# Kernel optimization log

Hardware: AMD Instinct MI355X
Metric: run time of the kernel (lower is better)

Reference implementation:

```python
import jax, jax.numpy as jnp
import numpy as np

TAU = 0.05
SIGMA = 0.05
THETA = 1.0
MAX_ITER = 30
B, N, M1, M2 = 8192, 256, 128, 64


def setup_inputs() -> dict:
    key = jax.random.key(0)
    k = jax.random.split(key, 5)
    x0 = jax.random.normal(k[0], (B, N), dtype=jnp.float32)
    y1_0 = jnp.zeros((B, M1), dtype=jnp.float32)
    y2_0 = jnp.zeros((B, M2), dtype=jnp.float32)
    z = jax.random.normal(k[1], (B, M1 + M2), dtype=jnp.float32)
    c = jax.random.normal(k[2], (N,), dtype=jnp.float32)
    # scale constraint matrices so tau*sigma*||A||^2 < 1 (PDHG stability)
    A1 = jax.random.normal(k[3], (M1, N), dtype=jnp.float32) * 0.1
    A2 = jax.random.normal(k[4], (M2, N), dtype=jnp.float32) * 0.1
    return {"x0": x0, "y1_0": y1_0, "y2_0": y2_0, "z": z, "c": c, "A1": A1, "A2": A2}


def reference(x0, y1_0, y2_0, z, c, A1, A2):
    # affine constraint maps: ineq_map(x, z) = x @ A1^T - z1 ; eq_map(x, z) = x @ A2^T - z2
    # adjoints: A1^T y1 = y1 @ A1 ; A2^T y2 = y2 @ A2
    # prox: projection onto nonnegative orthant
    z1, z2 = z[:, :M1], z[:, M1:]

    def step(carry, _):
        x, x_bar, y1, y2 = carry
        y1 = jnp.maximum(y1 + SIGMA * (x_bar @ A1.T - z1), 0.0)   # dual ineq ascent + clamp
        y2 = y2 + SIGMA * (x_bar @ A2.T - z2)                     # dual eq ascent
        grad = c + y1 @ A1 + y2 @ A2                              # [B, N] via broadcast of c
        x_next = jnp.maximum(x - TAU * grad, 0.0)                 # prox (nonneg projection)
        x_bar = x_next + THETA * (x_next - x)                     # extrapolation
        return (x_next, x_bar, y1, y2), None

    (x, _, y1, y2), _ = jax.lax.scan(step, (x0, x0, y1_0, y2_0), None, length=MAX_ITER)
    return (x, y1, y2)
```

## Files before the change

### kernel.cpp

```cpp
#include <hip/hip_runtime.h>

typedef __attribute__((ext_vector_type(8))) __bf16 bf16x8;
typedef __attribute__((ext_vector_type(4))) float f32x4;

constexpr int Bn = 8192, Nn = 256, M1n = 128, M2n = 64, Mn = 192, ITERS = 30;
constexpr float TAUc = 0.05f, SIGc = 0.05f;

__device__ __forceinline__ ushort f2bf(float f) {
  unsigned u = __builtin_bit_cast(unsigned, f);
  u = (u + 0x7FFFu + ((u >> 16) & 1u)) >> 16;
  return (ushort)u;
}

__global__ void prep_kernel(const float* __restrict__ A1, const float* __restrict__ A2,
                            ushort* __restrict__ Arm, ushort* __restrict__ AT) {
  int i = blockIdx.x * 256 + threadIdx.x;
  if (i >= Mn * Nn) return;
  int m = i / Nn, n = i % Nn;
  float v = (m < M1n) ? A1[m * Nn + n] : A2[(m - M1n) * Nn + n];
  ushort b = f2bf(v);
  Arm[m * Nn + n] = b;
  AT[n * Mn + m] = b;
}

__global__ __launch_bounds__(512, 2) void pdhg_kernel(
    const float* __restrict__ x0, const float* __restrict__ y10,
    const float* __restrict__ y20, const float* __restrict__ z,
    const float* __restrict__ c, const ushort* __restrict__ Arm,
    const ushort* __restrict__ AT, float* __restrict__ out) {
  __shared__ __align__(16) ushort xb_lds[16][264];
  __shared__ __align__(16) ushort y_lds[16][200];

  const int lane = threadIdx.x & 63;
  const int w = threadIdx.x >> 6;
  const int fr = lane & 15;
  const int kg = lane >> 4;
  const int row0 = blockIdx.x * 16;

  const int nt0 = 2 * w;
  const int mt0 = w;
  const bool two_m = (w < 4);
  const int mt1 = two_m ? (8 + w) : w;
  const int m0 = mt0 * 16 + fr;
  const int m1 = mt1 * 16 + fr;

  float x[2][4], cv[2];
  float y0s[4], z0s[4], y1s[4], z1s[4];

#pragma unroll
  for (int t = 0; t < 2; ++t) {
    int n = (nt0 + t) * 16 + fr;
    cv[t] = c[n];
#pragma unroll
    for (int g = 0; g < 4; ++g) {
      float v = x0[(row0 + kg * 4 + g) * Nn + n];
      x[t][g] = v;
      xb_lds[kg * 4 + g][n] = f2bf(v);
    }
  }
#pragma unroll
  for (int g = 0; g < 4; ++g) {
    int r = row0 + kg * 4 + g;
    z0s[g] = z[r * Mn + m0];
    y0s[g] = y10[r * M1n + m0];
    z1s[g] = z[r * Mn + m1];
    y1s[g] = two_m ? y20[r * M2n + (m1 - M1n)] : 0.f;
  }

  bf16x8 armF0[8], armF1[8], atF[2][6];
#pragma unroll
  for (int kf = 0; kf < 8; ++kf) {
    armF0[kf] = *reinterpret_cast<const bf16x8*>(&Arm[m0 * Nn + kf * 32 + kg * 8]);
    armF1[kf] = *reinterpret_cast<const bf16x8*>(&Arm[m1 * Nn + kf * 32 + kg * 8]);
  }
#pragma unroll
  for (int t = 0; t < 2; ++t)
#pragma unroll
    for (int kf = 0; kf < 6; ++kf)
      atF[t][kf] = *reinterpret_cast<const bf16x8*>(&AT[((nt0 + t) * 16 + fr) * Mn + kf * 32 + kg * 8]);

  __syncthreads();

  for (int it = 0; it < ITERS; ++it) {
    bf16x8 fx[8];
#pragma unroll
    for (int kf = 0; kf < 8; ++kf)
      fx[kf] = *reinterpret_cast<const bf16x8*>(&xb_lds[fr][kf * 32 + kg * 8]);

    f32x4 a0 = {0.f, 0.f, 0.f, 0.f}, a1 = {0.f, 0.f, 0.f, 0.f};
    if (two_m) {
#pragma unroll
      for (int kf = 0; kf < 8; ++kf) {
        a0 = __builtin_amdgcn_mfma_f32_16x16x32_bf16(fx[kf], armF0[kf], a0, 0, 0, 0);
        a1 = __builtin_amdgcn_mfma_f32_16x16x32_bf16(fx[kf], armF1[kf], a1, 0, 0, 0);
      }
    } else {
#pragma unroll
      for (int kf = 0; kf < 8; ++kf)
        a0 = __builtin_amdgcn_mfma_f32_16x16x32_bf16(fx[kf], armF0[kf], a0, 0, 0, 0);
    }

#pragma unroll
    for (int g = 0; g < 4; ++g) {
      float s = fmaxf(y0s[g] + SIGc * (a0[g] - z0s[g]), 0.f);
      y0s[g] = s;
      y_lds[kg * 4 + g][m0] = f2bf(s);
    }
    if (two_m) {
#pragma unroll
      for (int g = 0; g < 4; ++g) {
        float s = y1s[g] + SIGc * (a1[g] - z1s[g]);
        y1s[g] = s;
        y_lds[kg * 4 + g][m1] = f2bf(s);
      }
    }
    __syncthreads();

    bf16x8 fy[6];
#pragma unroll
    for (int kf = 0; kf < 6; ++kf)
      fy[kf] = *reinterpret_cast<const bf16x8*>(&y_lds[fr][kf * 32 + kg * 8]);

    f32x4 b0 = {0.f, 0.f, 0.f, 0.f}, b1 = {0.f, 0.f, 0.f, 0.f};
#pragma unroll
    for (int kf = 0; kf < 6; ++kf) {
      b0 = __builtin_amdgcn_mfma_f32_16x16x32_bf16(fy[kf], atF[0][kf], b0, 0, 0, 0);
      b1 = __builtin_amdgcn_mfma_f32_16x16x32_bf16(fy[kf], atF[1][kf], b1, 0, 0, 0);
    }

    const bool notlast = (it != ITERS - 1);
#pragma unroll
    for (int t = 0; t < 2; ++t) {
      int n = (nt0 + t) * 16 + fr;
      f32x4 bb = t ? b1 : b0;
#pragma unroll
      for (int g = 0; g < 4; ++g) {
        float grad = cv[t] + bb[g];
        float xn = fmaxf(x[t][g] - TAUc * grad, 0.f);
        float xb = 2.f * xn - x[t][g];
        x[t][g] = xn;
        if (notlast) xb_lds[kg * 4 + g][n] = f2bf(xb);
      }
    }
    __syncthreads();
  }

  float* ox = out;
  float* oy1 = out + Bn * Nn;
  float* oy2 = oy1 + Bn * M1n;
#pragma unroll
  for (int t = 0; t < 2; ++t) {
    int n = (nt0 + t) * 16 + fr;
#pragma unroll
    for (int g = 0; g < 4; ++g)
      ox[(row0 + kg * 4 + g) * Nn + n] = x[t][g];
  }
#pragma unroll
  for (int g = 0; g < 4; ++g) {
    int r = row0 + kg * 4 + g;
    oy1[r * M1n + m0] = y0s[g];
  }
  if (two_m) {
#pragma unroll
    for (int g = 0; g < 4; ++g) {
      int r = row0 + kg * 4 + g;
      oy2[r * M2n + (m1 - M1n)] = y1s[g];
    }
  }
}

extern "C" void kernel_launch(void* const* d_in, const int* in_sizes, int n_in,
                              void* d_out, int out_size, void* d_ws, size_t ws_size,
                              hipStream_t stream) {
  const float* x0  = (const float*)d_in[0];
  const float* y10 = (const float*)d_in[1];
  const float* y20 = (const float*)d_in[2];
  const float* z   = (const float*)d_in[3];
  const float* c   = (const float*)d_in[4];
  const float* A1  = (const float*)d_in[5];
  const float* A2  = (const float*)d_in[6];

  ushort* Arm = (ushort*)d_ws;
  ushort* AT  = Arm + Mn * Nn;

  prep_kernel<<<(Mn * Nn + 255) / 256, 256, 0, stream>>>(A1, A2, Arm, AT);
  pdhg_kernel<<<Bn / 16, 512, 0, stream>>>(x0, y10, y20, z, c, Arm, AT, (float*)d_out);
}
```

Baseline: 79.95 us.

## Use 4 waves per block with balanced MFMA tiles and packed bf16 conversion

```diff
diff --git a/kernel.cpp b/kernel.cpp
--- a/kernel.cpp
+++ b/kernel.cpp
@@ -12,6 +12,12 @@
   return (ushort)u;
 }
 
+__device__ __forceinline__ unsigned cvtpk(float lo, float hi) {
+  unsigned r;
+  asm("v_cvt_pk_bf16_f32 %0, %1, %2" : "=v"(r) : "v"(lo), "v"(hi));
+  return r;
+}
+
 __global__ void prep_kernel(const float* __restrict__ A1, const float* __restrict__ A2,
                             ushort* __restrict__ Arm, ushort* __restrict__ AT) {
   int i = blockIdx.x * 256 + threadIdx.x;
@@ -23,13 +29,14 @@
   AT[n * Mn + m] = b;
 }
 
-__global__ __launch_bounds__(512, 2) void pdhg_kernel(
+__global__ __launch_bounds__(256, 2) void pdhg_kernel(
     const float* __restrict__ x0, const float* __restrict__ y10,
     const float* __restrict__ y20, const float* __restrict__ z,
     const float* __restrict__ c, const ushort* __restrict__ Arm,
     const ushort* __restrict__ AT, float* __restrict__ out) {
   __shared__ __align__(16) ushort xb_lds[16][264];
   __shared__ __align__(16) ushort y_lds[16][200];
+  __shared__ __align__(16) float z_lds[16][200];
 
   const int lane = threadIdx.x & 63;
   const int w = threadIdx.x >> 6;
@@ -37,19 +44,16 @@
   const int kg = lane >> 4;
   const int row0 = blockIdx.x * 16;
 
-  const int nt0 = 2 * w;
-  const int mt0 = w;
-  const bool two_m = (w < 4);
-  const int mt1 = two_m ? (8 + w) : w;
-  const int m0 = mt0 * 16 + fr;
-  const int m1 = mt1 * 16 + fr;
+  for (int idx = threadIdx.x; idx < 16 * Mn; idx += 256) {
+    int r = idx / Mn, m = idx - r * Mn;
+    z_lds[r][m] = SIGc * z[(row0 + r) * Mn + m];
+  }
 
-  float x[2][4], cv[2];
-  float y0s[4], z0s[4], y1s[4], z1s[4];
+  float x[4][4], cv[4], ys[3][4];
 
 #pragma unroll
-  for (int t = 0; t < 2; ++t) {
-    int n = (nt0 + t) * 16 + fr;
+  for (int t = 0; t < 4; ++t) {
+    int n = (4 * w + t) * 16 + fr;
     cv[t] = c[n];
 #pragma unroll
     for (int g = 0; g < 4; ++g) {
@@ -59,112 +63,117 @@
     }
   }
 #pragma unroll
-  for (int g = 0; g < 4; ++g) {
-    int r = row0 + kg * 4 + g;
-    z0s[g] = z[r * Mn + m0];
-    y0s[g] = y10[r * M1n + m0];
-    z1s[g] = z[r * Mn + m1];
-    y1s[g] = two_m ? y20[r * M2n + (m1 - M1n)] : 0.f;
+  for (int i = 0; i < 3; ++i) {
+    int mt = 3 * w + i;
+    int m = mt * 16 + fr;
+#pragma unroll
+    for (int g = 0; g < 4; ++g) {
+      int r = row0 + kg * 4 + g;
+      ys[i][g] = (m < M1n) ? y10[r * M1n + m] : y20[r * M2n + (m - M1n)];
+    }
   }
 
-  bf16x8 armF0[8], armF1[8], atF[2][6];
+  bf16x8 armF[3][8], atF[4][6];
 #pragma unroll
-  for (int kf = 0; kf < 8; ++kf) {
-    armF0[kf] = *reinterpret_cast<const bf16x8*>(&Arm[m0 * Nn + kf * 32 + kg * 8]);
-    armF1[kf] = *reinterpret_cast<const bf16x8*>(&Arm[m1 * Nn + kf * 32 + kg * 8]);
+  for (int i = 0; i < 3; ++i) {
+    int m = (3 * w + i) * 16 + fr;
+#pragma unroll
+    for (int kf = 0; kf < 8; ++kf)
+      armF[i][kf] = *reinterpret_cast<const bf16x8*>(&Arm[m * Nn + kf * 32 + kg * 8]);
   }
 #pragma unroll
-  for (int t = 0; t < 2; ++t)
+  for (int t = 0; t < 4; ++t) {
+    int n = (4 * w + t) * 16 + fr;
 #pragma unroll
     for (int kf = 0; kf < 6; ++kf)
-      atF[t][kf] = *reinterpret_cast<const bf16x8*>(&AT[((nt0 + t) * 16 + fr) * Mn + kf * 32 + kg * 8]);
+      atF[t][kf] = *reinterpret_cast<const bf16x8*>(&AT[n * Mn + kf * 32 + kg * 8]);
+  }
 
   __syncthreads();
 
   for (int it = 0; it < ITERS; ++it) {
-    bf16x8 fx[8];
+    f32x4 a0 = {0.f, 0.f, 0.f, 0.f}, a1 = a0, a2 = a0;
 #pragma unroll
-    for (int kf = 0; kf < 8; ++kf)
-      fx[kf] = *reinterpret_cast<const bf16x8*>(&xb_lds[fr][kf * 32 + kg * 8]);
-
-    f32x4 a0 = {0.f, 0.f, 0.f, 0.f}, a1 = {0.f, 0.f, 0.f, 0.f};
-    if (two_m) {
-#pragma unroll
-      for (int kf = 0; kf < 8; ++kf) {
-        a0 = __builtin_amdgcn_mfma_f32_16x16x32_bf16(fx[kf], armF0[kf], a0, 0, 0, 0);
-        a1 = __builtin_amdgcn_mfma_f32_16x16x32_bf16(fx[kf], armF1[kf], a1, 0, 0, 0);
-      }
-    } else {
-#pragma unroll
-      for (int kf = 0; kf < 8; ++kf)
-        a0 = __builtin_amdgcn_mfma_f32_16x16x32_bf16(fx[kf], armF0[kf], a0, 0, 0, 0);
+    for (int kf = 0; kf < 8; ++kf) {
+      bf16x8 fx = *reinterpret_cast<const bf16x8*>(&xb_lds[fr][kf * 32 + kg * 8]);
+      a0 = __builtin_amdgcn_mfma_f32_16x16x32_bf16(fx, armF[0][kf], a0, 0, 0, 0);
+      a1 = __builtin_amdgcn_mfma_f32_16x16x32_bf16(fx, armF[1][kf], a1, 0, 0, 0);
+      a2 = __builtin_amdgcn_mfma_f32_16x16x32_bf16(fx, armF[2][kf], a2, 0, 0, 0);
     }
 
 #pragma unroll
-    for (int g = 0; g < 4; ++g) {
-      float s = fmaxf(y0s[g] + SIGc * (a0[g] - z0s[g]), 0.f);
-      y0s[g] = s;
-      y_lds[kg * 4 + g][m0] = f2bf(s);
-    }
-    if (two_m) {
+    for (int i = 0; i < 3; ++i) {
+      int mt = 3 * w + i;
+      int m = mt * 16 + fr;
+      const f32x4 ai = (i == 0) ? a0 : (i == 1) ? a1 : a2;
 #pragma unroll
       for (int g = 0; g < 4; ++g) {
-        float s = y1s[g] + SIGc * (a1[g] - z1s[g]);
-        y1s[g] = s;
-        y_lds[kg * 4 + g][m1] = f2bf(s);
+        float s = __builtin_fmaf(SIGc, ai[g], ys[i][g]) - z_lds[kg * 4 + g][m];
+        if (mt < 8) s = fmaxf(s, 0.f);
+        ys[i][g] = s;
       }
+      unsigned p01 = cvtpk(ys[i][0], ys[i][1]);
+      unsigned p23 = cvtpk(ys[i][2], ys[i][3]);
+      y_lds[kg * 4 + 0][m] = (ushort)p01;
+      y_lds[kg * 4 + 1][m] = (ushort)(p01 >> 16);
+      y_lds[kg * 4 + 2][m] = (ushort)p23;
+      y_lds[kg * 4 + 3][m] = (ushort)(p23 >> 16);
     }
     __syncthreads();
 
-    bf16x8 fy[6];
-#pragma unroll
-    for (int kf = 0; kf < 6; ++kf)
-      fy[kf] = *reinterpret_cast<const bf16x8*>(&y_lds[fr][kf * 32 + kg * 8]);
-
-    f32x4 b0 = {0.f, 0.f, 0.f, 0.f}, b1 = {0.f, 0.f, 0.f, 0.f};
+    f32x4 b0 = {0.f, 0.f, 0.f, 0.f}, b1 = b0, b2 = b0, b3 = b0;
 #pragma unroll
     for (int kf = 0; kf < 6; ++kf) {
-      b0 = __builtin_amdgcn_mfma_f32_16x16x32_bf16(fy[kf], atF[0][kf], b0, 0, 0, 0);
-      b1 = __builtin_amdgcn_mfma_f32_16x16x32_bf16(fy[kf], atF[1][kf], b1, 0, 0, 0);
+      bf16x8 fy = *reinterpret_cast<const bf16x8*>(&y_lds[fr][kf * 32 + kg * 8]);
+      b0 = __builtin_amdgcn_mfma_f32_16x16x32_bf16(fy, atF[0][kf], b0, 0, 0, 0);
+      b1 = __builtin_amdgcn_mfma_f32_16x16x32_bf16(fy, atF[1][kf], b1, 0, 0, 0);
+      b2 = __builtin_amdgcn_mfma_f32_16x16x32_bf16(fy, atF[2][kf], b2, 0, 0, 0);
+      b3 = __builtin_amdgcn_mfma_f32_16x16x32_bf16(fy, atF[3][kf], b3, 0, 0, 0);
     }
 
     const bool notlast = (it != ITERS - 1);
 #pragma unroll
-    for (int t = 0; t < 2; ++t) {
-      int n = (nt0 + t) * 16 + fr;
-      f32x4 bb = t ? b1 : b0;
+    for (int t = 0; t < 4; ++t) {
+      int n = (4 * w + t) * 16 + fr;
+      const f32x4 bt = (t == 0) ? b0 : (t == 1) ? b1 : (t == 2) ? b2 : b3;
+      float xb[4];
 #pragma unroll
       for (int g = 0; g < 4; ++g) {
-        float grad = cv[t] + bb[g];
-        float xn = fmaxf(x[t][g] - TAUc * grad, 0.f);
-        float xb = 2.f * xn - x[t][g];
+        float grad = cv[t] + bt[g];
+        float xn = fmaxf(__builtin_fmaf(-TAUc, grad, x[t][g]), 0.f);
+        xb[g] = 2.f * xn - x[t][g];
         x[t][g] = xn;
-        if (notlast) xb_lds[kg * 4 + g][n] = f2bf(xb);
+      }
+      if (notlast) {
+        unsigned p01 = cvtpk(xb[0], xb[1]);
+        unsigned p23 = cvtpk(xb[2], xb[3]);
+        xb_lds[kg * 4 + 0][n] = (ushort)p01;
+        xb_lds[kg * 4 + 1][n] = (ushort)(p01 >> 16);
+        xb_lds[kg * 4 + 2][n] = (ushort)p23;
+        xb_lds[kg * 4 + 3][n] = (ushort)(p23 >> 16);
       }
     }
-    __syncthreads();
+    if (notlast) __syncthreads();
   }
 
   float* ox = out;
   float* oy1 = out + Bn * Nn;
   float* oy2 = oy1 + Bn * M1n;
 #pragma unroll
-  for (int t = 0; t < 2; ++t) {
-    int n = (nt0 + t) * 16 + fr;
+  for (int t = 0; t < 4; ++t) {
+    int n = (4 * w + t) * 16 + fr;
 #pragma unroll
     for (int g = 0; g < 4; ++g)
       ox[(row0 + kg * 4 + g) * Nn + n] = x[t][g];
   }
 #pragma unroll
-  for (int g = 0; g < 4; ++g) {
-    int r = row0 + kg * 4 + g;
-    oy1[r * M1n + m0] = y0s[g];
-  }
-  if (two_m) {
+  for (int i = 0; i < 3; ++i) {
+    int m = (3 * w + i) * 16 + fr;
 #pragma unroll
     for (int g = 0; g < 4; ++g) {
       int r = row0 + kg * 4 + g;
-      oy2[r * M2n + (m1 - M1n)] = y1s[g];
+      if (m < M1n) oy1[r * M1n + m] = ys[i][g];
+      else         oy2[r * M2n + (m - M1n)] = ys[i][g];
     }
   }
 }
@@ -184,5 +193,5 @@
   ushort* AT  = Arm + Mn * Nn;
 
   prep_kernel<<<(Mn * Nn + 255) / 256, 256, 0, stream>>>(A1, A2, Arm, AT);
-  pdhg_kernel<<<Bn / 16, 512, 0, stream>>>(x0, y10, y20, z, c, Arm, AT, (float*)d_out);
+  pdhg_kernel<<<Bn / 16, 256, 0, stream>>>(x0, y10, y20, z, c, Arm, AT, (float*)d_out);
 }
```

After: 81.81 us. +2.3%, slower.
